# Kernel optimization log

Hardware: AMD Instinct MI355X
Metric: run time of the kernel (lower is better)

## Reference

```python
import jax, jax.numpy as jnp
import numpy as np

B, N, C, D, O = 32, 512, 16, 256, 256


def setup_inputs() -> dict:
    key = jax.random.key(0)
    k1, k2, k3, k4, k5, k6 = jax.random.split(key, 6)
    std = 1.0 / np.sqrt(D)
    nodes = jax.random.normal(k1, (B, N, D), jnp.float32)
    children = jax.random.randint(k2, (B, N, C), 0, N)  # 0 == no-child sentinel
    w_t = jax.random.normal(k3, (D, O), jnp.float32) * std
    w_l = jax.random.normal(k4, (D, O), jnp.float32) * std
    w_r = jax.random.normal(k5, (D, O), jnp.float32) * std
    conv = jax.random.normal(k6, (O,), jnp.float32) * np.sqrt(2.0 / D)
    return {"nodes": nodes, "w_t": w_t, "w_l": w_l, "w_r": w_r, "conv": conv,
            "children": children}


def _coefs(children):
    # children: (B, N, C) int. Returns coef (B, N, C+1, 3) = stack(c_t, c_r, c_l).
    b, n, c = children.shape
    y = c + 1
    has_child = jnp.minimum(children, 1).astype(jnp.float32)          # (B,N,C)
    mask = jnp.concatenate([jnp.zeros((b, n, 1), jnp.float32), has_child], axis=2)  # (B,N,Y)
    # eta_t: 1 at slot 0 (parent), 0 elsewhere
    c_t = jnp.concatenate([jnp.ones((b, n, 1), jnp.float32),
                           jnp.zeros((b, n, c), jnp.float32)], axis=2)
    # eta_r
    ns = jnp.count_nonzero(children, axis=2).astype(jnp.float32)[..., None]  # (B,N,1)
    p = jnp.arange(-1.0, c, dtype=jnp.float32)                        # (Y,): -1,0,1,...
    child_idx = p * mask                                              # (B,N,Y)
    singles = (jnp.arange(y) == 1).astype(jnp.float32) * 0.5          # (Y,)
    denom = jnp.where(ns == 1.0, 1.0, ns - 1.0)                       # safe divide
    c_r = jnp.where(ns == 1.0,
                    jnp.broadcast_to(singles, mask.shape),
                    (1.0 - c_t) * (child_idx / denom))
    # eta_l
    c_l = (1.0 - c_t) * (1.0 - c_r) * mask
    return jnp.stack([c_t, c_r, c_l], axis=3)                         # (B,N,Y,3)


def reference(nodes, w_t, w_l, w_r, conv, children):
    b, n, d = nodes.shape
    c = children.shape[2]
    # gather children embeddings: child_emb[b,i,j] = nodes[b, children[b,i,j]]
    flat_idx = children.reshape(b, n * c)
    child_emb = jnp.take_along_axis(nodes, flat_idx[:, :, None], axis=1)
    child_emb = child_emb.reshape(b, n, c, d)
    child_emb = jnp.where((children == 0)[..., None], 0.0, child_emb)
    tree = jnp.concatenate([nodes[:, :, None, :], child_emb], axis=2)  # (B,N,Y,D)
    coef = _coefs(children)                                            # (B,N,Y,3)
    weights = jnp.stack([w_t, w_r, w_l], axis=0)                       # (3,D,O)
    agg = jnp.einsum('bnyd,bnyk->bnkd', tree, coef)                    # (B,N,3,D)
    res = jnp.einsum('bnkd,kdo->bno', agg, weights)                    # (B,N,O)
    return jax.nn.leaky_relu(res + conv, negative_slope=0.01)
```

## Files before the change

### kernel.cpp

```cpp
#include <hip/hip_runtime.h>
#include <hip/hip_bf16.h>
#include <stdint.h>

#define CC 16
#define OO 256
#define NSLAB 24
#define MT_ROWS 64
#define SLAB_ELS (MT_ROWS * 32)
#define MT_ELS (NSLAB * SLAB_ELS)
#define AGG_ELS (16384 * 768)
#define NGB 2048

typedef __attribute__((ext_vector_type(8))) short bf16x8;
typedef __attribute__((ext_vector_type(4))) float f32x4;

__device__ __forceinline__ unsigned short f2bf(float x) {
    unsigned u = __builtin_bit_cast(unsigned, x);
    u += 0x7FFFu + ((u >> 16) & 1u);
    return (unsigned short)(u >> 16);
}

__device__ __forceinline__ void st_bf4(unsigned short* p, float4 v) {
    uint2 u;
    u.x = (unsigned)f2bf(v.x) | ((unsigned)f2bf(v.y) << 16);
    u.y = (unsigned)f2bf(v.z) | ((unsigned)f2bf(v.w) << 16);
    *(uint2*)p = u;
}

__device__ __forceinline__ void cp16(const void* g, void* l) {
    __builtin_amdgcn_global_load_lds(
        (const __attribute__((address_space(1))) unsigned int*)g,
        (__attribute__((address_space(3))) unsigned int*)l, 16, 0, 0);
}

__global__ __launch_bounds__(256, 4) void gather_prep(
    const float* __restrict__ nodes, const int* __restrict__ children,
    const float* __restrict__ wt, const float* __restrict__ wrp,
    const float* __restrict__ wl, unsigned short* __restrict__ agg,
    unsigned short* __restrict__ wsb) {

    __shared__ unsigned short T[256 * 40];
    const int p = blockIdx.x;
    const int tid = threadIdx.x;

    if (p >= NGB) {
        const int slab = p - NGB;
        const int n = tid;
#pragma unroll
        for (int kk = 0; kk < 32; ++kk) {
            const int k = slab * 32 + kk;
            const float* s = (k < 256) ? wt : ((k < 512) ? wrp : wl);
            T[n * 40 + kk] = f2bf(s[(k & 255) * OO + n]);
        }
        __syncthreads();
        uint4* dst = (uint4*)(wsb + slab * 8192 + n * 32);
        const uint4* src = (const uint4*)&T[n * 40];
#pragma unroll
        for (int q = 0; q < 4; ++q) dst[q] = src[q];
        return;
    }

    const int wave = tid >> 6;
    const int lane = tid & 63;
    const int lb = (p & 7) * 256 + (p >> 3);
    const int base = lb * 8;
    const float4* g4 = (const float4*)nodes;

#pragma unroll 1
    for (int i = 0; i < 2; ++i) {
        const int nf = __builtin_amdgcn_readfirstlane(base + wave * 2 + i);
        const int brow = nf & ~511;
        const int* chp = children + (nf << 4);
        int cj[CC];
#pragma unroll
        for (int j = 0; j < CC; ++j) cj[j] = chp[j];
        int ns = 0;
#pragma unroll
        for (int j = 0; j < CC; ++j) ns += (cj[j] != 0) ? 1 : 0;
        const float inv_den = (ns > 1) ? 1.0f / (float)(ns - 1) : 0.0f;
        const bool single = (ns == 1);

        float4 pt = g4[(size_t)nf * 64 + lane];
        float4 e[CC];
#pragma unroll
        for (int j = 0; j < CC; ++j)
            e[j] = g4[(size_t)(brow + cj[j]) * 64 + lane];

        float4 ar = make_float4(0.f, 0.f, 0.f, 0.f);
        float4 al = make_float4(0.f, 0.f, 0.f, 0.f);
#pragma unroll
        for (int j = 0; j < CC; ++j) {
            const float hasf = (cj[j] != 0) ? 1.0f : 0.0f;
            const float crr_raw = single ? ((j == 0) ? 0.5f : 0.0f)
                                         : (float)j * inv_den;
            const float cr = crr_raw * hasf;
            const float cl = (1.0f - crr_raw) * hasf;
            ar.x += cr * e[j].x; ar.y += cr * e[j].y;
            ar.z += cr * e[j].z; ar.w += cr * e[j].w;
            al.x += cl * e[j].x; al.y += cl * e[j].y;
            al.z += cl * e[j].z; al.w += cl * e[j].w;
        }
        const int sl = lane >> 3;
        const int kw = (lane & 7) * 4;
        unsigned short* rowp = agg + (size_t)(nf >> 6) * MT_ELS
                                   + (size_t)(nf & 63) * 32 + kw;
        st_bf4(rowp + (size_t)(0  + sl) * SLAB_ELS, pt);
        st_bf4(rowp + (size_t)(8  + sl) * SLAB_ELS, ar);
        st_bf4(rowp + (size_t)(16 + sl) * SLAB_ELS, al);
    }
}

__global__ __launch_bounds__(256, 2) void gemm_ep(
    const unsigned short* __restrict__ agg, const unsigned short* __restrict__ wsb,
    const float* __restrict__ conv, float* __restrict__ out) {

    __shared__ unsigned short Ab[2][SLAB_ELS];
    __shared__ unsigned short Bb[2][4096];

    const int tid  = threadIdx.x;
    const int wave = tid >> 6;
    const int lane = tid & 63;
    const int quad = lane >> 4;
    const int l16  = lane & 15;
    const int mtile = blockIdx.x >> 1;
    const int ntile = blockIdx.x & 1;
    const int wrr = wave >> 1;
    const int wcc = wave & 1;

    const char* aggb = (const char*)agg + (size_t)mtile * (MT_ELS * 2);
    const char* wsbb = (const char*)wsb + ntile * 8192;
    const int toff  = tid * 16;
    const int wbase = (tid & ~63) * 16;

    f32x4 acc[2][4];
#pragma unroll
    for (int mi = 0; mi < 2; ++mi)
#pragma unroll
        for (int ni = 0; ni < 4; ++ni)
            acc[mi][ni] = (f32x4){0.f, 0.f, 0.f, 0.f};

    auto stage = [&](int s, int b) {
        const char* ga = aggb + s * 4096 + toff;
        cp16(ga, (char*)&Ab[b][0] + wbase);
        const char* gb = wsbb + s * 16384 + toff;
        cp16(gb,        (char*)&Bb[b][0] + wbase);
        cp16(gb + 4096, (char*)&Bb[b][0] + wbase + 4096);
    };

    stage(0, 0);
#pragma unroll 1
    for (int s = 0; s < NSLAB; ++s) {
        const int cur = s & 1;
        __syncthreads();
        if (s + 1 < NSLAB) stage(s + 1, cur ^ 1);

        bf16x8 af[2], bfr[4];
#pragma unroll
        for (int mi = 0; mi < 2; ++mi)
            af[mi] = *(const bf16x8*)&Ab[cur][(wrr * 32 + mi * 16 + l16) * 32 + quad * 8];
#pragma unroll
        for (int ni = 0; ni < 4; ++ni)
            bfr[ni] = *(const bf16x8*)&Bb[cur][(wcc * 64 + ni * 16 + l16) * 32 + quad * 8];
#pragma unroll
        for (int mi = 0; mi < 2; ++mi)
#pragma unroll
            for (int ni = 0; ni < 4; ++ni)
                acc[mi][ni] = __builtin_amdgcn_mfma_f32_16x16x32_bf16(
                    af[mi], bfr[ni], acc[mi][ni], 0, 0, 0);
    }

#pragma unroll
    for (int ni = 0; ni < 4; ++ni) {
        const int col = ntile * 128 + wcc * 64 + ni * 16 + l16;
        const float cv = conv[col];
#pragma unroll
        for (int mi = 0; mi < 2; ++mi) {
#pragma unroll
            for (int r = 0; r < 4; ++r) {
                const int row = mtile * 64 + wrr * 32 + mi * 16 + quad * 4 + r;
                float v = acc[mi][ni][r] + cv;
                v = (v > 0.f) ? v : 0.01f * v;
                out[(size_t)row * OO + col] = v;
            }
        }
    }
}

extern "C" void kernel_launch(void* const* d_in, const int* in_sizes, int n_in,
                              void* d_out, int out_size, void* d_ws, size_t ws_size,
                              hipStream_t stream) {
    const float* nodes    = (const float*)d_in[0];
    const float* w_t      = (const float*)d_in[1];
    const float* w_l      = (const float*)d_in[2];
    const float* w_r      = (const float*)d_in[3];
    const float* conv     = (const float*)d_in[4];
    const int*   children = (const int*)d_in[5];

    unsigned short* agg = (unsigned short*)d_ws;
    unsigned short* wsb = agg + AGG_ELS;

    gather_prep<<<NGB + 24, 256, 0, stream>>>(nodes, children, w_t, w_r, w_l,
                                              agg, wsb);
    gemm_ep<<<512, 256, 0, stream>>>(agg, wsb, conv, (float*)d_out);
}
```

Measured before the change: 105.7 us.

## Pre-convert nodes to bf16 and gather children from compact bf16 copy

```diff
diff --git a/kernel.cpp b/kernel.cpp
--- a/kernel.cpp
+++ b/kernel.cpp
@@ -5,11 +5,10 @@
 #define CC 16
 #define OO 256
 #define NSLAB 24
-#define MT_ROWS 64
-#define SLAB_ELS (MT_ROWS * 32)
+#define SLAB_ELS 2048
 #define MT_ELS (NSLAB * SLAB_ELS)
 #define AGG_ELS (16384 * 768)
-#define NGB 2048
+#define NB_ELS  (16384 * 256)
 
 typedef __attribute__((ext_vector_type(8))) short bf16x8;
 typedef __attribute__((ext_vector_type(4))) float f32x4;
@@ -33,81 +32,93 @@
         (__attribute__((address_space(3))) unsigned int*)l, 16, 0, 0);
 }
 
-__global__ __launch_bounds__(256, 4) void gather_prep(
-    const float* __restrict__ nodes, const int* __restrict__ children,
-    const float* __restrict__ wt, const float* __restrict__ wrp,
-    const float* __restrict__ wl, unsigned short* __restrict__ agg,
-    unsigned short* __restrict__ wsb) {
+__global__ __launch_bounds__(256) void prep(
+    const float* __restrict__ nodes, const float* __restrict__ wt,
+    const float* __restrict__ wrp, const float* __restrict__ wl,
+    unsigned short* __restrict__ nb, unsigned short* __restrict__ wsb) {
 
     __shared__ unsigned short T[256 * 40];
     const int p = blockIdx.x;
     const int tid = threadIdx.x;
 
-    if (p >= NGB) {
-        const int slab = p - NGB;
-        const int n = tid;
-#pragma unroll
-        for (int kk = 0; kk < 32; ++kk) {
-            const int k = slab * 32 + kk;
-            const float* s = (k < 256) ? wt : ((k < 512) ? wrp : wl);
-            T[n * 40 + kk] = f2bf(s[(k & 255) * OO + n]);
-        }
-        __syncthreads();
-        uint4* dst = (uint4*)(wsb + slab * 8192 + n * 32);
-        const uint4* src = (const uint4*)&T[n * 40];
-#pragma unroll
-        for (int q = 0; q < 4; ++q) dst[q] = src[q];
+    if (p < 2048) {
+        const size_t t = (size_t)p * 256 + tid;
+        const float4* s = (const float4*)nodes + t * 2;
+        float4 a = s[0], b = s[1];
+        uint4 u;
+        u.x = (unsigned)f2bf(a.x) | ((unsigned)f2bf(a.y) << 16);
+        u.y = (unsigned)f2bf(a.z) | ((unsigned)f2bf(a.w) << 16);
+        u.z = (unsigned)f2bf(b.x) | ((unsigned)f2bf(b.y) << 16);
+        u.w = (unsigned)f2bf(b.z) | ((unsigned)f2bf(b.w) << 16);
+        *(uint4*)(nb + t * 8) = u;
         return;
     }
-
-    const int wave = tid >> 6;
-    const int lane = tid & 63;
-    const int lb = (p & 7) * 256 + (p >> 3);
-    const int base = lb * 8;
+    const int slab = p - 2048;
+    const int n = tid;
+#pragma unroll
+    for (int kk = 0; kk < 32; ++kk) {
+        const int k = slab * 32 + kk;
+        const float* s = (k < 256) ? wt : ((k < 512) ? wrp : wl);
+        T[n * 40 + kk] = f2bf(s[(k & 255) * OO + n]);
+    }
+    __syncthreads();
+    uint4* dst = (uint4*)(wsb + slab * 8192 + n * 32);
+    const uint4* src = (const uint4*)&T[n * 40];
+#pragma unroll
+    for (int q = 0; q < 4; ++q) dst[q] = src[q];
+}
+
+__global__ __launch_bounds__(256, 8) void gather(
+    const float* __restrict__ nodes, const unsigned short* __restrict__ nb,
+    const int* __restrict__ children, unsigned short* __restrict__ agg) {
+
+    const int wave = threadIdx.x >> 6;
+    const int lane = threadIdx.x & 63;
+    const int p = blockIdx.x;
+    const int g = (p & 7) * 512 + (p >> 3);
+    const int nf = __builtin_amdgcn_readfirstlane(g * 4 + wave);
+    const int brow = nf & ~511;
+
+    const int* chp = children + (nf << 4);
+    int cj[CC];
+#pragma unroll
+    for (int j = 0; j < CC; ++j) cj[j] = chp[j];
+    int ns = 0;
+#pragma unroll
+    for (int j = 0; j < CC; ++j) ns += (cj[j] != 0) ? 1 : 0;
+    const float inv_den = (ns > 1) ? 1.0f / (float)(ns - 1) : 0.0f;
+    const bool single = (ns == 1);
+
     const float4* g4 = (const float4*)nodes;
-
-#pragma unroll 1
-    for (int i = 0; i < 2; ++i) {
-        const int nf = __builtin_amdgcn_readfirstlane(base + wave * 2 + i);
-        const int brow = nf & ~511;
-        const int* chp = children + (nf << 4);
-        int cj[CC];
-#pragma unroll
-        for (int j = 0; j < CC; ++j) cj[j] = chp[j];
-        int ns = 0;
-#pragma unroll
-        for (int j = 0; j < CC; ++j) ns += (cj[j] != 0) ? 1 : 0;
-        const float inv_den = (ns > 1) ? 1.0f / (float)(ns - 1) : 0.0f;
-        const bool single = (ns == 1);
-
-        float4 pt = g4[(size_t)nf * 64 + lane];
-        float4 e[CC];
-#pragma unroll
-        for (int j = 0; j < CC; ++j)
-            e[j] = g4[(size_t)(brow + cj[j]) * 64 + lane];
-
-        float4 ar = make_float4(0.f, 0.f, 0.f, 0.f);
-        float4 al = make_float4(0.f, 0.f, 0.f, 0.f);
-#pragma unroll
-        for (int j = 0; j < CC; ++j) {
-            const float hasf = (cj[j] != 0) ? 1.0f : 0.0f;
-            const float crr_raw = single ? ((j == 0) ? 0.5f : 0.0f)
-                                         : (float)j * inv_den;
-            const float cr = crr_raw * hasf;
-            const float cl = (1.0f - crr_raw) * hasf;
-            ar.x += cr * e[j].x; ar.y += cr * e[j].y;
-            ar.z += cr * e[j].z; ar.w += cr * e[j].w;
-            al.x += cl * e[j].x; al.y += cl * e[j].y;
-            al.z += cl * e[j].z; al.w += cl * e[j].w;
-        }
-        const int sl = lane >> 3;
-        const int kw = (lane & 7) * 4;
-        unsigned short* rowp = agg + (size_t)(nf >> 6) * MT_ELS
-                                   + (size_t)(nf & 63) * 32 + kw;
-        st_bf4(rowp + (size_t)(0  + sl) * SLAB_ELS, pt);
-        st_bf4(rowp + (size_t)(8  + sl) * SLAB_ELS, ar);
-        st_bf4(rowp + (size_t)(16 + sl) * SLAB_ELS, al);
-    }
+    float4 pt = g4[(size_t)nf * 64 + lane];
+    uint2 ec[CC];
+#pragma unroll
+    for (int j = 0; j < CC; ++j)
+        ec[j] = *(const uint2*)(nb + ((size_t)(brow + cj[j]) << 8) + (lane << 2));
+
+    float4 ar = make_float4(0.f, 0.f, 0.f, 0.f);
+    float4 al = make_float4(0.f, 0.f, 0.f, 0.f);
+#pragma unroll
+    for (int j = 0; j < CC; ++j) {
+        const float hasf = (cj[j] != 0) ? 1.0f : 0.0f;
+        const float crr = single ? ((j == 0) ? 0.5f : 0.0f) : (float)j * inv_den;
+        const float cr = crr * hasf;
+        const float cl = (1.0f - crr) * hasf;
+        const float e0 = __builtin_bit_cast(float, ec[j].x << 16);
+        const float e1 = __builtin_bit_cast(float, ec[j].x & 0xFFFF0000u);
+        const float e2 = __builtin_bit_cast(float, ec[j].y << 16);
+        const float e3 = __builtin_bit_cast(float, ec[j].y & 0xFFFF0000u);
+        ar.x += cr * e0; ar.y += cr * e1; ar.z += cr * e2; ar.w += cr * e3;
+        al.x += cl * e0; al.y += cl * e1; al.z += cl * e2; al.w += cl * e3;
+    }
+
+    const int sl  = lane >> 3;
+    const int kwb = (lane & 7) * 4;
+    unsigned short* rowp = agg + (size_t)(nf >> 6) * MT_ELS
+                               + (size_t)(nf & 63) * 32 + kwb;
+    st_bf4(rowp + (size_t)(0  + sl) * SLAB_ELS, pt);
+    st_bf4(rowp + (size_t)(8  + sl) * SLAB_ELS, ar);
+    st_bf4(rowp + (size_t)(16 + sl) * SLAB_ELS, al);
 }
 
 __global__ __launch_bounds__(256, 2) void gemm_ep(
@@ -122,8 +133,10 @@
     const int lane = tid & 63;
     const int quad = lane >> 4;
     const int l16  = lane & 15;
-    const int mtile = blockIdx.x >> 1;
-    const int ntile = blockIdx.x & 1;
+    const int x = blockIdx.x & 7;
+    const int q = blockIdx.x >> 3;
+    const int mtile = x * 32 + (q >> 1);
+    const int ntile = q & 1;
     const int wrr = wave >> 1;
     const int wcc = wave & 1;
 
@@ -198,8 +211,9 @@
 
     unsigned short* agg = (unsigned short*)d_ws;
     unsigned short* wsb = agg + AGG_ELS;
-
-    gather_prep<<<NGB + 24, 256, 0, stream>>>(nodes, children, w_t, w_r, w_l,
-                                              agg, wsb);
+    unsigned short* nbb = wsb + 768 * 256;
+
+    prep<<<2048 + 24, 256, 0, stream>>>(nodes, w_t, w_r, w_l, nbb, wsb);
+    gather<<<4096, 256, 0, stream>>>(nodes, nbb, children, agg);
     gemm_ep<<<512, 256, 0, stream>>>(agg, wsb, conv, (float*)d_out);
 }
```

New measurement: 111.0 us. +5.1%, slower.
